# Kernel tuning notes

Measured on AMD Instinct MI355X. Metric: run time of the kernel, lower is better.

The kernel has to match this reference:

```python
import jax, jax.numpy as jnp
import numpy as np

B, S, HIDDEN, H, KVH, D = 4, 1024, 4096, 32, 8, 128
ROT = D // 2  # rotary_dim = head_size/2 (inv_freq over arange(0, dim, 2))
NUM_SLOTS = 8192
ROPE_THETA = 10000.0


def setup_inputs() -> dict:
    key = jax.random.key(0)
    k0, k1, k2 = jax.random.split(key, 3)
    T = B * S
    hidden_states = jax.random.normal(k0, (T, HIDDEN), dtype=jnp.float32) * 0.02
    # RoPE tables: positions 0..S-1 per sequence, gathered per token, shape [T,1,ROT]
    inv_freq = 1.0 / (ROPE_THETA ** (np.arange(0, D, 2, dtype=np.float32) / D))
    pos = jnp.tile(jnp.arange(S, dtype=jnp.float32), B)          # [T]
    freqs = pos[:, None] * jnp.asarray(inv_freq)[None, :]        # [T, ROT]
    cos = jnp.cos(freqs)[:, None, :]
    sin = jnp.sin(freqs)[:, None, :]
    w_qkv = jax.random.normal(k1, (H * D + 2 * KVH * D, HIDDEN), dtype=jnp.float32) * 0.02
    w_o = jax.random.normal(k2, (HIDDEN, H * D), dtype=jnp.float32) * 0.02
    slots = jnp.arange(T, dtype=jnp.int32)
    key_cache = jnp.zeros((NUM_SLOTS, KVH, D), dtype=jnp.float32)
    value_cache = jnp.zeros((NUM_SLOTS, KVH, D), dtype=jnp.float32)
    return {"hidden_states": hidden_states, "cos": cos, "sin": sin,
            "w_qkv": w_qkv, "w_o": w_o,
            "key_cache": key_cache, "value_cache": value_cache,
            "slots": slots, "seq_len": S}


def _rope(x, cos, sin):
    # x: [T, heads, D]; cos/sin: [T, 1, ROT]; NeoX half-split rotation
    x1, x2 = x[..., :ROT], x[..., ROT:2 * ROT]
    return jnp.concatenate([x1 * cos - x2 * sin, x1 * sin + x2 * cos], axis=-1)


def reference(hidden_states, cos, sin, w_qkv, w_o, key_cache, value_cache, slots, seq_len):
    T, hidden = hidden_states.shape
    kvh = key_cache.shape[1]
    d = key_cache.shape[2]
    h = (w_qkv.shape[0] - 2 * kvh * d) // d
    b = T // seq_len
    groups = h // kvh
    scale = d ** -0.5

    # fused QKV projection
    qkv = hidden_states @ w_qkv.T                              # [T, (h+2*kvh)*d]
    q = qkv[:, : h * d].reshape(T, h, d)
    k = qkv[:, h * d: h * d + kvh * d].reshape(T, kvh, d)
    v = qkv[:, h * d + kvh * d:].reshape(T, kvh, d)

    # in-place RoPE on query and key
    q = _rope(q, cos, sin)
    k = _rope(k, cos, sin)

    # reshape_and_cache: scatter rotated K and V into slot-indexed cache
    new_key_cache = key_cache.at[slots].set(k)
    new_value_cache = value_cache.at[slots].set(v)

    # prefill varlen flash attention (equal-length sequences), causal, GQA
    qb = q.reshape(b, seq_len, h, d)
    kb = jnp.repeat(k.reshape(b, seq_len, kvh, d), groups, axis=2)  # [b,s,h,d]
    vb = jnp.repeat(v.reshape(b, seq_len, kvh, d), groups, axis=2)
    scores = jnp.einsum('bqhd,bkhd->bhqk', qb, kb) * scale
    causal = jnp.tril(jnp.ones((seq_len, seq_len), dtype=bool))
    scores = jnp.where(causal[None, None], scores, jnp.finfo(scores.dtype).min)
    attn = jax.nn.softmax(scores, axis=-1)
    out = jnp.einsum('bhqk,bkhd->bqhd', attn, vb).reshape(T, h * d)

    return out @ w_o.T, new_key_cache, new_value_cache
```

## Files before the change

kernel.cpp:

```cpp
#include <hip/hip_runtime.h>
#include <hip/hip_bf16.h>

#define B_    4
#define S_    1024
#define HID   4096
#define H_    32
#define KVH_  8
#define D_    128
#define T_    (B_ * S_)
#define QKVD  (H_ * D_ + 2 * KVH_ * D_)
#define NSLOT 8192

typedef __attribute__((ext_vector_type(8))) short short8;
typedef __attribute__((ext_vector_type(4))) float f32x4;

#define MFMA_B16(d, x, y) \
  d = __builtin_amdgcn_mfma_f32_16x16x32_bf16(x, y, d, 0, 0, 0)

__device__ __forceinline__ unsigned short f2b(float f) {
  union { __hip_bfloat16 h; unsigned short u; } c;
  c.h = __float2bfloat16(f);
  return c.u;
}
__device__ __forceinline__ float b2f(unsigned short u) {
  union { unsigned int i; float f; } c;
  c.i = ((unsigned int)u) << 16;
  return c.f;
}

__device__ __forceinline__ void async16(const void* g, void* l) {
  __builtin_amdgcn_global_load_lds(
      (const __attribute__((address_space(1))) unsigned int*)g,
      (__attribute__((address_space(3))) unsigned int*)l,
      16, 0, 0);
}

__global__ void conv_bf16(const float* __restrict__ src,
                          unsigned short* __restrict__ dst, int n4) {
  int i = blockIdx.x * 256 + threadIdx.x;
  if (i >= n4) return;
  float4 v = reinterpret_cast<const float4*>(src)[i];
  ushort4 o;
  o.x = f2b(v.x); o.y = f2b(v.y); o.z = f2b(v.z); o.w = f2b(v.w);
  reinterpret_cast<ushort4*>(dst)[i] = o;
}

template <bool BF16OUT>
__global__ __launch_bounds__(512, 2) void gemm_bt(
    const unsigned short* __restrict__ A, const unsigned short* __restrict__ Bm,
    void* __restrict__ Cv, int M, int N, int K) {
  __shared__ unsigned short As[2 * 2 * 256 * 32];
  __shared__ unsigned short Bs[2 * 2 * 256 * 32];
  const int tid  = threadIdx.x;
  const int lane = tid & 63;
  const int w    = tid >> 6;
  const int quad = lane >> 4;
  const int l16  = lane & 15;
  const int bm = blockIdx.y * 256;
  const int bn = blockIdx.x * 256;
  const int wm = (w >> 2) * 128;
  const int wn = (w & 3) * 64;

  const int r0 = tid >> 2;
  const int c0 = ((tid & 3) ^ ((r0 >> 1) & 3)) * 8;
  const unsigned short* Ag = A + (size_t)(bm + r0) * K + c0;
  const unsigned short* Bg = Bm + (size_t)(bn + r0) * K + c0;
  const size_t rstep = (size_t)128 * K;

  const int qoff = (quad ^ ((l16 >> 1) & 3)) * 8;
  const int aro = (wm + l16) * 32 + qoff;
  const int bro = (wn + l16) * 32 + qoff;

  f32x4 acc[8][4];
#pragma unroll
  for (int f = 0; f < 8; f++)
#pragma unroll
    for (int c = 0; c < 4; c++)
#pragma unroll
      for (int r = 0; r < 4; r++) acc[f][c][r] = 0.f;

  unsigned short* lA = As + tid * 8;
  unsigned short* lB = Bs + tid * 8;

  async16(Ag,              lA);
  async16(Ag + rstep,      lA + 4096);
  async16(Bg,              lB);
  async16(Bg + rstep,      lB + 4096);
  async16(Ag + 32,         lA + 8192);
  async16(Ag + rstep + 32, lA + 8192 + 4096);
  async16(Bg + 32,         lB + 8192);
  async16(Bg + rstep + 32, lB + 8192 + 4096);

  const int KT = K >> 6;
  for (int kt = 0; kt < KT; ++kt) {
    const int cur = (kt & 1) << 14;
    const int nxt = cur ^ 16384;
    const size_t knx = (size_t)((kt + 1 < KT) ? (kt + 1) : kt) << 6;
    const unsigned short* Ac = As + cur;
    const unsigned short* Bc = Bs + cur;
    unsigned short* An = As + nxt + tid * 8;
    unsigned short* Bn = Bs + nxt + tid * 8;
    short8 a[8], b0, b1;

    async16(Ag + knx,         An);
    async16(Ag + knx + rstep, An + 4096);
    asm volatile("s_waitcnt vmcnt(4)" ::: "memory");
    __builtin_amdgcn_s_barrier();
#pragma unroll
    for (int f = 0; f < 8; f++) a[f] = *(const short8*)(Ac + f * 512 + aro);
    b0 = *(const short8*)(Bc + bro);
    b1 = *(const short8*)(Bc + 512 + bro);
    __builtin_amdgcn_s_setprio(1);
#pragma unroll
    for (int f = 0; f < 8; f++) MFMA_B16(acc[f][0], a[f], b0);
#pragma unroll
    for (int f = 0; f < 8; f++) MFMA_B16(acc[f][1], a[f], b1);
    __builtin_amdgcn_s_setprio(0);

    async16(Bg + knx,         Bn);
    async16(Bg + knx + rstep, Bn + 4096);
    b0 = *(const short8*)(Bc + 1024 + bro);
    b1 = *(const short8*)(Bc + 1536 + bro);
    __builtin_amdgcn_s_setprio(1);
#pragma unroll
    for (int f = 0; f < 8; f++) MFMA_B16(acc[f][2], a[f], b0);
#pragma unroll
    for (int f = 0; f < 8; f++) MFMA_B16(acc[f][3], a[f], b1);
    __builtin_amdgcn_s_setprio(0);

    async16(Ag + knx + 32,         An + 8192);
    async16(Ag + knx + 32 + rstep, An + 8192 + 4096);
    asm volatile("s_waitcnt vmcnt(4)" ::: "memory");
    __builtin_amdgcn_s_barrier();
#pragma unroll
    for (int f = 0; f < 8; f++) a[f] = *(const short8*)(Ac + 8192 + f * 512 + aro);
    b0 = *(const short8*)(Bc + 8192 + bro);
    b1 = *(const short8*)(Bc + 8192 + 512 + bro);
    __builtin_amdgcn_s_setprio(1);
#pragma unroll
    for (int f = 0; f < 8; f++) MFMA_B16(acc[f][0], a[f], b0);
#pragma unroll
    for (int f = 0; f < 8; f++) MFMA_B16(acc[f][1], a[f], b1);
    __builtin_amdgcn_s_setprio(0);

    async16(Bg + knx + 32,         Bn + 8192);
    async16(Bg + knx + 32 + rstep, Bn + 8192 + 4096);
    b0 = *(const short8*)(Bc + 8192 + 1024 + bro);
    b1 = *(const short8*)(Bc + 8192 + 1536 + bro);
    __builtin_amdgcn_s_setprio(1);
#pragma unroll
    for (int f = 0; f < 8; f++) MFMA_B16(acc[f][2], a[f], b0);
#pragma unroll
    for (int f = 0; f < 8; f++) MFMA_B16(acc[f][3], a[f], b1);
    __builtin_amdgcn_s_setprio(0);
  }
  asm volatile("s_waitcnt vmcnt(0)" ::: "memory");

  const int crow0 = bm + wm + quad * 4;
  const int ccol0 = bn + wn + l16;
  if constexpr (BF16OUT) {
    unsigned short* C = (unsigned short*)Cv;
#pragma unroll
    for (int f = 0; f < 8; f++)
#pragma unroll
      for (int c = 0; c < 4; c++)
#pragma unroll
        for (int r = 0; r < 4; r++)
          C[(size_t)(crow0 + f * 16 + r) * N + ccol0 + c * 16] = f2b(acc[f][c][r]);
  } else {
    float* C = (float*)Cv;
#pragma unroll
    for (int f = 0; f < 8; f++)
#pragma unroll
      for (int c = 0; c < 4; c++)
#pragma unroll
        for (int r = 0; r < 4; r++)
          C[(size_t)(crow0 + f * 16 + r) * N + ccol0 + c * 16] = acc[f][c][r];
  }
}

__global__ void rope_scatter(
    const unsigned short* __restrict__ qkv, const float* __restrict__ cosb,
    const float* __restrict__ sinb, const int* __restrict__ slots,
    unsigned short* __restrict__ qb, unsigned short* __restrict__ kb,
    unsigned short* __restrict__ vb, float* __restrict__ kco,
    float* __restrict__ vco) {
  const float sl2 = 0.08838834764831843f * 1.4426950408889634f;
  const int t = blockIdx.x;
  const int tid = threadIdx.x;
  const int b = t >> 10, s = t & 1023;
  const unsigned short* row = qkv + (size_t)t * QKVD;
  const float* cs = cosb + (size_t)t * 64;
  const float* sn = sinb + (size_t)t * 64;
  const int slot = slots[t];
  for (int wk = tid; wk < H_ * 64; wk += 256) {
    int hh = wk >> 6, i = wk & 63;
    float x1 = b2f(row[hh * D_ + i]), x2 = b2f(row[hh * D_ + 64 + i]);
    float c = cs[i], sv = sn[i];
    size_t base = ((size_t)(b * H_ + hh) * S_ + s) * D_;
    qb[base + i]      = f2b((x1 * c - x2 * sv) * sl2);
    qb[base + 64 + i] = f2b((x1 * sv + x2 * c) * sl2);
  }
  for (int wk = tid; wk < KVH_ * 64; wk += 256) {
    int hh = wk >> 6, i = wk & 63;
    float x1 = b2f(row[H_ * D_ + hh * D_ + i]);
    float x2 = b2f(row[H_ * D_ + hh * D_ + 64 + i]);
    float c = cs[i], sv = sn[i];
    float o1 = x1 * c - x2 * sv, o2 = x1 * sv + x2 * c;
    size_t base = ((size_t)(b * KVH_ + hh) * S_ + s) * D_;
    kb[base + i] = f2b(o1);
    kb[base + 64 + i] = f2b(o2);
    size_t cb = ((size_t)slot * KVH_ + hh) * D_;
    kco[cb + i] = o1;
    kco[cb + 64 + i] = o2;
  }
  for (int wk = tid; wk < KVH_ * D_; wk += 256) {
    int hh = wk >> 7, i = wk & 127;
    unsigned short xv = row[H_ * D_ + KVH_ * D_ + hh * D_ + i];
    vb[((size_t)(b * KVH_ + hh) * S_ + s) * D_ + i] = xv;
    vco[((size_t)slot * KVH_ + hh) * D_ + i] = b2f(xv);
  }
}

__global__ void transpose_v(const unsigned short* __restrict__ vb,
                            unsigned short* __restrict__ vt) {
  __shared__ unsigned short tile[64][65];
  const int bid = blockIdx.x;
  const int dt = bid & 1, st = (bid >> 1) & 15, bk = bid >> 5;
  const int tid = threadIdx.x;
  const unsigned short* src = vb + ((size_t)bk * S_ + st * 64) * D_ + dt * 64;
#pragma unroll
  for (int k = 0; k < 16; k++) {
    int e = k * 256 + tid, r = e >> 6, c = e & 63;
    tile[r][c] = src[(size_t)r * D_ + c];
  }
  __syncthreads();
  unsigned short* dst = vt + ((size_t)bk * D_ + dt * 64) * S_ + st * 64;
#pragma unroll
  for (int k = 0; k < 16; k++) {
    int e = k * 256 + tid, r = e >> 6, c = e & 63;
    dst[(size_t)r * S_ + c] = tile[c][r];
  }
}

__global__ __launch_bounds__(256) void attn_fused(
    const unsigned short* __restrict__ qb, const unsigned short* __restrict__ kb,
    const unsigned short* __restrict__ vt, unsigned short* __restrict__ ob) {
  __shared__ unsigned short Ks[4 * 64 * 32];
  __shared__ unsigned short Vs[2 * 128 * 32];
  __shared__ unsigned short Ps[4][2 * 16 * 32];
  const int tid = threadIdx.x;
  const int lane = tid & 63, w = tid >> 6;
  const int quad = lane >> 4, l16 = lane & 15;
  const int bidx = blockIdx.x;
  const int qt = 15 - (bidx & 15);
  const int bh = bidx >> 4;
  const int h = bh & 31, b = bh >> 5;
  const int kvh = h >> 2;
  const int q0 = qt * 64;
  const unsigned short* qbase = qb + ((size_t)bh * S_ + q0) * D_;
  const unsigned short* kbase = kb + (size_t)(b * KVH_ + kvh) * S_ * D_;
  const unsigned short* vbase = vt + (size_t)(b * KVH_ + kvh) * D_ * S_;

  const int srow = tid >> 2;
  const int scol = (((tid & 3) ^ ((tid >> 3) & 3)) * 8);
  const int qoff = (quad ^ ((l16 >> 1) & 3)) * 8;

#pragma unroll
  for (int i = 0; i < 4; i++)
    async16(qbase + (size_t)srow * D_ + i * 32 + scol, (unsigned short*)Ks + i * 2048 + tid * 8);
  __syncthreads();
  short8 qf[4];
#pragma unroll
  for (int kc = 0; kc < 4; kc++)
    qf[kc] = *(const short8*)(Ks + (kc * 64 + w * 16 + l16) * 32 + qoff);

  short8 of;
  {
    unsigned short ov = (l16 == 0) ? (unsigned short)0x3F80 : (unsigned short)0;
#pragma unroll
    for (int j = 0; j < 8; j++) of[j] = (short)ov;
  }

  f32x4 oac[8];
  f32x4 osum;
#pragma unroll
  for (int n = 0; n < 8; n++)
#pragma unroll
    for (int r = 0; r < 4; r++) oac[n][r] = 0.f;
#pragma unroll
  for (int r = 0; r < 4; r++) osum[r] = 0.f;
  float m_run[4] = {-3.0e38f, -3.0e38f, -3.0e38f, -3.0e38f};

  unsigned short* psw = &Ps[w][0];
  const int qrow = q0 + w * 16 + quad * 4;

  for (int jt = 0; jt <= qt; jt++) {
    __syncthreads();
    const int j0 = jt * 64;
#pragma unroll
    for (int i = 0; i < 4; i++)
      async16(kbase + (size_t)(j0 + srow) * D_ + i * 32 + scol,
              (unsigned short*)Ks + i * 2048 + tid * 8);
#pragma unroll
    for (int i = 0; i < 4; i++) {
      int kc = i >> 1;
      int d = (i & 1) * 64 + srow;
      async16(vbase + (size_t)d * S_ + j0 + kc * 32 + scol,
              (unsigned short*)Vs + i * 2048 + tid * 8);
    }
    __syncthreads();

    f32x4 sac[4];
#pragma unroll
    for (int t = 0; t < 4; t++)
#pragma unroll
      for (int r = 0; r < 4; r++) sac[t][r] = 0.f;
#pragma unroll
    for (int t = 0; t < 4; t++)
#pragma unroll
      for (int kc = 0; kc < 4; kc++)
        sac[t] = __builtin_amdgcn_mfma_f32_16x16x32_bf16(
            qf[kc], *(const short8*)(Ks + (kc * 64 + t * 16 + l16) * 32 + qoff),
            sac[t], 0, 0, 0);

    if (jt == qt) {
#pragma unroll
      for (int t = 0; t < 4; t++) {
        const int kcol = j0 + t * 16 + l16;
#pragma unroll
        for (int r = 0; r < 4; r++)
          if (kcol > qrow + r) sac[t][r] = -3.0e38f;
      }
    }
    float mx[4];
#pragma unroll
    for (int r = 0; r < 4; r++)
      mx[r] = fmaxf(fmaxf(sac[0][r], sac[1][r]), fmaxf(sac[2][r], sac[3][r]));
#pragma unroll
    for (int off = 1; off < 16; off <<= 1)
#pragma unroll
      for (int r = 0; r < 4; r++) mx[r] = fmaxf(mx[r], __shfl_xor(mx[r], off));
    float alpha[4];
#pragma unroll
    for (int r = 0; r < 4; r++) {
      float mn = fmaxf(m_run[r], mx[r]);
      alpha[r] = exp2f(m_run[r] - mn);
      m_run[r] = mn;
    }
#pragma unroll
    for (int t = 0; t < 4; t++)
#pragma unroll
      for (int r = 0; r < 4; r++) {
        float p = exp2f(sac[t][r] - m_run[r]);
        int prow = quad * 4 + r;
        int chunk = (((t & 1) * 2 + (l16 >> 3)) ^ ((prow >> 1) & 3));
        psw[(t >> 1) * 512 + prow * 32 + chunk * 8 + (l16 & 7)] = f2b(p);
      }
#pragma unroll
    for (int r = 0; r < 4; r++) osum[r] *= alpha[r];
#pragma unroll
    for (int n = 0; n < 8; n++)
#pragma unroll
      for (int r = 0; r < 4; r++) oac[n][r] *= alpha[r];
#pragma unroll
    for (int kc = 0; kc < 2; kc++) {
      short8 pf = *(const short8*)(psw + kc * 512 + l16 * 32 + qoff);
      osum = __builtin_amdgcn_mfma_f32_16x16x32_bf16(pf, of, osum, 0, 0, 0);
#pragma unroll
      for (int n = 0; n < 8; n++)
        oac[n] = __builtin_amdgcn_mfma_f32_16x16x32_bf16(
            pf, *(const short8*)(Vs + (kc * 128 + n * 16 + l16) * 32 + qoff),
            oac[n], 0, 0, 0);
    }
  }

  float inv[4];
#pragma unroll
  for (int r = 0; r < 4; r++) {
    float l = __shfl(osum[r], lane & 48, 64);
    inv[r] = 1.0f / l;
  }
  const size_t trow = (size_t)(b * S_ + q0 + w * 16 + quad * 4);
#pragma unroll
  for (int n = 0; n < 8; n++)
#pragma unroll
    for (int r = 0; r < 4; r++)
      ob[(trow + r) * (size_t)(H_ * D_) + h * D_ + n * 16 + l16] =
          f2b(oac[n][r] * inv[r]);
}

extern "C" void kernel_launch(void* const* d_in, const int* in_sizes, int n_in,
                              void* d_out, int out_size, void* d_ws, size_t ws_size,
                              hipStream_t stream) {
  const float* hidden = (const float*)d_in[0];
  const float* cosb   = (const float*)d_in[1];
  const float* sinb   = (const float*)d_in[2];
  const float* wqkv   = (const float*)d_in[3];
  const float* wo     = (const float*)d_in[4];
  const float* kc_in  = (const float*)d_in[5];
  const float* vc_in  = (const float*)d_in[6];
  const int*   slots  = (const int*)d_in[7];

  float* out    = (float*)d_out;
  float* kc_out = out + (size_t)T_ * HID;
  float* vc_out = kc_out + (size_t)NSLOT * KVH_ * D_;

  char* ws = (char*)d_ws;
  unsigned short* hb    = (unsigned short*)ws; ws += (size_t)T_ * HID * 2;
  unsigned short* wqkvb = (unsigned short*)ws; ws += (size_t)QKVD * HID * 2;
  unsigned short* wob   = (unsigned short*)ws; ws += (size_t)HID * HID * 2;
  unsigned short* qkv   = (unsigned short*)ws; ws += (size_t)T_ * QKVD * 2;
  unsigned short* qb    = (unsigned short*)ws; ws += (size_t)T_ * H_ * D_ * 2;
  unsigned short* kb    = (unsigned short*)ws; ws += (size_t)T_ * KVH_ * D_ * 2;
  unsigned short* vb    = (unsigned short*)ws; ws += (size_t)T_ * KVH_ * D_ * 2;
  unsigned short* vt    = (unsigned short*)ws; ws += (size_t)T_ * KVH_ * D_ * 2;
  unsigned short* ob    = (unsigned short*)ws;

  const size_t cache_bytes = (size_t)NSLOT * KVH_ * D_ * 4;
  hipMemcpyAsync(kc_out, kc_in, cache_bytes, hipMemcpyDeviceToDevice, stream);
  hipMemcpyAsync(vc_out, vc_in, cache_bytes, hipMemcpyDeviceToDevice, stream);

  conv_bf16<<<(T_ * HID / 4) / 256, 256, 0, stream>>>(hidden, hb, T_ * HID / 4);
  conv_bf16<<<(QKVD * HID / 4) / 256, 256, 0, stream>>>(wqkv, wqkvb, QKVD * HID / 4);
  conv_bf16<<<(HID * HID / 4) / 256, 256, 0, stream>>>(wo, wob, HID * HID / 4);

  dim3 g1(QKVD / 256, T_ / 256);
  gemm_bt<true><<<g1, 512, 0, stream>>>(hb, wqkvb, qkv, T_, QKVD, HID);

  rope_scatter<<<T_, 256, 0, stream>>>(qkv, cosb, sinb, slots, qb, kb, vb, kc_out, vc_out);

  transpose_v<<<B_ * KVH_ * 16 * 2, 256, 0, stream>>>(vb, vt);

  attn_fused<<<B_ * H_ * (S_ / 64), 256, 0, stream>>>(qb, kb, vt, ob);

  dim3 g2(HID / 256, T_ / 256);
  gemm_bt<false><<<g2, 512, 0, stream>>>(ob, wob, out, T_, HID, HID);
}
```

Baseline: 973.1 us.

## Restructure GEMM shared-memory layout to 64-wide K tiles with finer staged pipeline

Rewrites the bf16 GEMM main loop so each shared-memory tile holds 64 K-elements per row (128-row halves) with an 8-way XOR swizzle instead of two 32-wide K slices. The K loop is split into four phases that each load fragments, issue one async half-tile copy for the next stage, barrier, then run MFMAs, with sched_barrier fences. The goal is to spread global-to-LDS traffic more evenly across the MFMA work and cut LDS bank conflicts. The cost is more barriers per iteration and a more delicate buffer-reuse order, where a race would corrupt results.

Result: no change. 989.2 us (+1.7%).

```diff
diff --git a/kernel.cpp b/kernel.cpp
--- a/kernel.cpp
+++ b/kernel.cpp
@@ -49,8 +49,8 @@
 __global__ __launch_bounds__(512, 2) void gemm_bt(
     const unsigned short* __restrict__ A, const unsigned short* __restrict__ Bm,
     void* __restrict__ Cv, int M, int N, int K) {
-  __shared__ unsigned short As[2 * 2 * 256 * 32];
-  __shared__ unsigned short Bs[2 * 2 * 256 * 32];
+  __shared__ unsigned short As[2 * 2 * 128 * 64];
+  __shared__ unsigned short Bs[2 * 2 * 128 * 64];
   const int tid  = threadIdx.x;
   const int lane = tid & 63;
   const int w    = tid >> 6;
@@ -58,18 +58,20 @@
   const int l16  = lane & 15;
   const int bm = blockIdx.y * 256;
   const int bn = blockIdx.x * 256;
-  const int wm = (w >> 2) * 128;
-  const int wn = (w & 3) * 64;
-
-  const int r0 = tid >> 2;
-  const int c0 = ((tid & 3) ^ ((r0 >> 1) & 3)) * 8;
-  const unsigned short* Ag = A + (size_t)(bm + r0) * K + c0;
-  const unsigned short* Bg = Bm + (size_t)(bn + r0) * K + c0;
-  const size_t rstep = (size_t)128 * K;
-
-  const int qoff = (quad ^ ((l16 >> 1) & 3)) * 8;
-  const int aro = (wm + l16) * 32 + qoff;
-  const int bro = (wn + l16) * 32 + qoff;
+  const int wmh = w >> 2;
+  const int wn  = (w & 3) * 64;
+  const int hB  = (w & 3) >> 1;
+
+  const int rr  = tid >> 3;
+  const int gch = ((tid & 7) ^ (rr & 7)) * 8;
+  const unsigned short* gA = A + (size_t)(bm + rr) * K + gch;
+  const unsigned short* gB = Bm + (size_t)(bn + rr) * K + gch;
+  const size_t r64 = (size_t)64 * K;
+
+  const int cp0 = ((quad) ^ (l16 & 7)) * 8;
+  const int cp1 = ((4 + quad) ^ (l16 & 7)) * 8;
+  const int abase = wmh * 8192 + l16 * 64;
+  const int bbase = hB * 8192 + ((w & 1) * 64 + l16) * 64;
 
   f32x4 acc[8][4];
 #pragma unroll
@@ -79,84 +81,122 @@
 #pragma unroll
       for (int r = 0; r < 4; r++) acc[f][c][r] = 0.f;
 
-  unsigned short* lA = As + tid * 8;
-  unsigned short* lB = Bs + tid * 8;
-
-  async16(Ag,              lA);
-  async16(Ag + rstep,      lA + 4096);
-  async16(Bg,              lB);
-  async16(Bg + rstep,      lB + 4096);
-  async16(Ag + 32,         lA + 8192);
-  async16(Ag + rstep + 32, lA + 8192 + 4096);
-  async16(Bg + 32,         lB + 8192);
-  async16(Bg + rstep + 32, lB + 8192 + 4096);
+  auto stageA = [&](int tau, int h, int buf) {
+    const unsigned short* s = gA + (size_t)(h * 2) * r64 + (size_t)tau * 64;
+    unsigned short* d = As + buf * 16384 + h * 8192 + tid * 8;
+    async16(s, d);
+    async16(s + r64, d + 4096);
+  };
+  auto stageB = [&](int tau, int h, int buf) {
+    const unsigned short* s = gB + (size_t)(h * 2) * r64 + (size_t)tau * 64;
+    unsigned short* d = Bs + buf * 16384 + h * 8192 + tid * 8;
+    async16(s, d);
+    async16(s + r64, d + 4096);
+  };
+
+  stageA(0, 0, 0);
+  stageA(0, 1, 0);
+  stageB(0, 0, 0);
+  stageB(0, 1, 0);
+  stageA(1, 0, 1);
+  asm volatile("s_waitcnt vmcnt(2)" ::: "memory");
+  __builtin_amdgcn_s_barrier();
 
   const int KT = K >> 6;
-  for (int kt = 0; kt < KT; ++kt) {
-    const int cur = (kt & 1) << 14;
-    const int nxt = cur ^ 16384;
-    const size_t knx = (size_t)((kt + 1 < KT) ? (kt + 1) : kt) << 6;
-    const unsigned short* Ac = As + cur;
-    const unsigned short* Bc = Bs + cur;
-    unsigned short* An = As + nxt + tid * 8;
-    unsigned short* Bn = Bs + nxt + tid * 8;
-    short8 a[8], b0, b1;
-
-    async16(Ag + knx,         An);
-    async16(Ag + knx + rstep, An + 4096);
-    asm volatile("s_waitcnt vmcnt(4)" ::: "memory");
-    __builtin_amdgcn_s_barrier();
-#pragma unroll
-    for (int f = 0; f < 8; f++) a[f] = *(const short8*)(Ac + f * 512 + aro);
-    b0 = *(const short8*)(Bc + bro);
-    b1 = *(const short8*)(Bc + 512 + bro);
+  short8 a[4][2], b[2][2];
+  for (int t = 0; t < KT; ++t) {
+    const int cb = t & 1, nb = cb ^ 1;
+    const int tn1 = (t + 1 < KT) ? t + 1 : KT - 1;
+    const int tn2 = (t + 2 < KT) ? t + 2 : KT - 1;
+    const unsigned short* Ab = As + cb * 16384 + abase;
+    const unsigned short* Bb = Bs + cb * 16384 + bbase;
+
+#pragma unroll
+    for (int f = 0; f < 4; f++) {
+      a[f][0] = *(const short8*)(Ab + f * 1024 + cp0);
+      a[f][1] = *(const short8*)(Ab + f * 1024 + cp1);
+    }
+    b[0][0] = *(const short8*)(Bb + cp0);
+    b[0][1] = *(const short8*)(Bb + cp1);
+    b[1][0] = *(const short8*)(Bb + 1024 + cp0);
+    b[1][1] = *(const short8*)(Bb + 1024 + cp1);
+    stageA(tn1, 1, nb);
+    __builtin_amdgcn_sched_barrier(0);
+    __builtin_amdgcn_s_barrier();
     __builtin_amdgcn_s_setprio(1);
 #pragma unroll
-    for (int f = 0; f < 8; f++) MFMA_B16(acc[f][0], a[f], b0);
-#pragma unroll
-    for (int f = 0; f < 8; f++) MFMA_B16(acc[f][1], a[f], b1);
+    for (int f = 0; f < 4; f++) {
+      MFMA_B16(acc[f][0], a[f][0], b[0][0]);
+      MFMA_B16(acc[f][0], a[f][1], b[0][1]);
+      MFMA_B16(acc[f][1], a[f][0], b[1][0]);
+      MFMA_B16(acc[f][1], a[f][1], b[1][1]);
+    }
     __builtin_amdgcn_s_setprio(0);
-
-    async16(Bg + knx,         Bn);
-    async16(Bg + knx + rstep, Bn + 4096);
-    b0 = *(const short8*)(Bc + 1024 + bro);
-    b1 = *(const short8*)(Bc + 1536 + bro);
+    __builtin_amdgcn_s_barrier();
+
+    b[0][0] = *(const short8*)(Bb + 2048 + cp0);
+    b[0][1] = *(const short8*)(Bb + 2048 + cp1);
+    b[1][0] = *(const short8*)(Bb + 3072 + cp0);
+    b[1][1] = *(const short8*)(Bb + 3072 + cp1);
+    stageB(tn1, 0, nb);
+    __builtin_amdgcn_sched_barrier(0);
+    __builtin_amdgcn_s_barrier();
     __builtin_amdgcn_s_setprio(1);
 #pragma unroll
-    for (int f = 0; f < 8; f++) MFMA_B16(acc[f][2], a[f], b0);
-#pragma unroll
-    for (int f = 0; f < 8; f++) MFMA_B16(acc[f][3], a[f], b1);
+    for (int f = 0; f < 4; f++) {
+      MFMA_B16(acc[f][2], a[f][0], b[0][0]);
+      MFMA_B16(acc[f][2], a[f][1], b[0][1]);
+      MFMA_B16(acc[f][3], a[f][0], b[1][0]);
+      MFMA_B16(acc[f][3], a[f][1], b[1][1]);
+    }
     __builtin_amdgcn_s_setprio(0);
-
-    async16(Ag + knx + 32,         An + 8192);
-    async16(Ag + knx + 32 + rstep, An + 8192 + 4096);
-    asm volatile("s_waitcnt vmcnt(4)" ::: "memory");
-    __builtin_amdgcn_s_barrier();
-#pragma unroll
-    for (int f = 0; f < 8; f++) a[f] = *(const short8*)(Ac + 8192 + f * 512 + aro);
-    b0 = *(const short8*)(Bc + 8192 + bro);
-    b1 = *(const short8*)(Bc + 8192 + 512 + bro);
+    __builtin_amdgcn_s_barrier();
+
+#pragma unroll
+    for (int f = 0; f < 4; f++) {
+      a[f][0] = *(const short8*)(Ab + 4096 + f * 1024 + cp0);
+      a[f][1] = *(const short8*)(Ab + 4096 + f * 1024 + cp1);
+    }
+    b[0][0] = *(const short8*)(Bb + cp0);
+    b[0][1] = *(const short8*)(Bb + cp1);
+    b[1][0] = *(const short8*)(Bb + 1024 + cp0);
+    b[1][1] = *(const short8*)(Bb + 1024 + cp1);
+    stageB(tn1, 1, nb);
+    __builtin_amdgcn_sched_barrier(0);
+    __builtin_amdgcn_s_barrier();
     __builtin_amdgcn_s_setprio(1);
 #pragma unroll
-    for (int f = 0; f < 8; f++) MFMA_B16(acc[f][0], a[f], b0);
-#pragma unroll
-    for (int f = 0; f < 8; f++) MFMA_B16(acc[f][1], a[f], b1);
+    for (int f = 0; f < 4; f++) {
+      MFMA_B16(acc[4 + f][0], a[f][0], b[0][0]);
+      MFMA_B16(acc[4 + f][0], a[f][1], b[0][1]);
+      MFMA_B16(acc[4 + f][1], a[f][0], b[1][0]);
+      MFMA_B16(acc[4 + f][1], a[f][1], b[1][1]);
+    }
     __builtin_amdgcn_s_setprio(0);
-
-    async16(Bg + knx + 32,         Bn + 8192);
-    async16(Bg + knx + 32 + rstep, Bn + 8192 + 4096);
-    b0 = *(const short8*)(Bc + 8192 + 1024 + bro);
-    b1 = *(const short8*)(Bc + 8192 + 1536 + bro);
+    __builtin_amdgcn_s_barrier();
+
+    b[0][0] = *(const short8*)(Bb + 2048 + cp0);
+    b[0][1] = *(const short8*)(Bb + 2048 + cp1);
+    b[1][0] = *(const short8*)(Bb + 3072 + cp0);
+    b[1][1] = *(const short8*)(Bb + 3072 + cp1);
+    stageA(tn2, 0, cb);
+    asm volatile("s_waitcnt vmcnt(2)" ::: "memory");
+    __builtin_amdgcn_sched_barrier(0);
+    __builtin_amdgcn_s_barrier();
     __builtin_amdgcn_s_setprio(1);
 #pragma unroll
-    for (int f = 0; f < 8; f++) MFMA_B16(acc[f][2], a[f], b0);
-#pragma unroll
-    for (int f = 0; f < 8; f++) MFMA_B16(acc[f][3], a[f], b1);
+    for (int f = 0; f < 4; f++) {
+      MFMA_B16(acc[4 + f][2], a[f][0], b[0][0]);
+      MFMA_B16(acc[4 + f][2], a[f][1], b[0][1]);
+      MFMA_B16(acc[4 + f][3], a[f][0], b[1][0]);
+      MFMA_B16(acc[4 + f][3], a[f][1], b[1][1]);
+    }
     __builtin_amdgcn_s_setprio(0);
+    __builtin_amdgcn_s_barrier();
   }
   asm volatile("s_waitcnt vmcnt(0)" ::: "memory");
 
-  const int crow0 = bm + wm + quad * 4;
+  const int crow0 = bm + wmh * 128 + quad * 4;
   const int ccol0 = bn + wn + l16;
   if constexpr (BF16OUT) {
     unsigned short* C = (unsigned short*)Cv;
```
